# Optimization experiments

Hardware: AMD Instinct MI355X
Metric: run time of the kernel (lower is better)

The kernel has to match this reference:

```python
import jax, jax.numpy as jnp
import numpy as np

WIN = 11      # pytorch_msssim default win_size
SIGMA = 1.5   # pytorch_msssim default win_sigma
K1, K2 = 0.01, 0.03
DATA_RANGE = 1.0


def _gauss_win():
    coords = np.arange(WIN, dtype=np.float64) - WIN // 2
    g = np.exp(-(coords ** 2) / (2.0 * SIGMA ** 2))
    g = g / g.sum()
    return jnp.asarray(g, dtype=jnp.float32)


def _gauss_filter(x, w):
    # x: [B, C, H, W]; separable depthwise gaussian, VALID padding (pytorch_msssim style)
    C = x.shape[1]
    dn = ('NCHW', 'OIHW', 'NCHW')
    kh = jnp.broadcast_to(w.reshape(1, 1, WIN, 1), (C, 1, WIN, 1))
    kw = jnp.broadcast_to(w.reshape(1, 1, 1, WIN), (C, 1, 1, WIN))
    x = jax.lax.conv_general_dilated(x, kh, (1, 1), 'VALID',
                                     dimension_numbers=dn, feature_group_count=C)
    x = jax.lax.conv_general_dilated(x, kw, (1, 1), 'VALID',
                                     dimension_numbers=dn, feature_group_count=C)
    return x


def _ssim_mean(X, Y):
    C1 = (K1 * DATA_RANGE) ** 2
    C2 = (K2 * DATA_RANGE) ** 2
    w = _gauss_win()
    mu1 = _gauss_filter(X, w)
    mu2 = _gauss_filter(Y, w)
    mu1_sq = mu1 * mu1
    mu2_sq = mu2 * mu2
    mu1_mu2 = mu1 * mu2
    sigma1_sq = _gauss_filter(X * X, w) - mu1_sq
    sigma2_sq = _gauss_filter(Y * Y, w) - mu2_sq
    sigma12 = _gauss_filter(X * Y, w) - mu1_mu2
    cs_map = (2.0 * sigma12 + C2) / (sigma1_sq + sigma2_sq + C2)
    ssim_map = ((2.0 * mu1_mu2 + C1) / (mu1_sq + mu2_sq + C1)) * cs_map
    return jnp.mean(ssim_map)


def setup_inputs() -> dict:
    key = jax.random.key(0)
    k1, k2 = jax.random.split(key)
    inp = jax.random.uniform(k1, (64, 1, 512, 512), dtype=jnp.float32)
    tgt = jax.random.uniform(k2, (64, 1, 512, 512), dtype=jnp.float32)
    return {"input": inp, "target": tgt}


def reference(input, target):
    # SSIMLoss.forward: 1 - SSIM(data_range=1, size_average=True, channel=1)(input, target)
    return 1.0 - _ssim_mean(input, target)
```

## Files before the change

kernel.cpp:

```cpp
#include <hip/hip_runtime.h>
#include <math.h>

#define WIN 11
#define OH 32
#define OW 54
#define IWV 64
#define VSTRH 64
#define PLANEH (OH * VSTRH)
#define IMG 512
#define OUTD 502
#define NIMG 64
#define NTX 10

typedef float    f32x2 __attribute__((ext_vector_type(2)));
typedef _Float16 h2    __attribute__((ext_vector_type(2)));
typedef _Float16 h8    __attribute__((ext_vector_type(8)));

struct GW {
    float    wf[WIN];
    unsigned whp[WIN];
};

__device__ inline h2 wsplat(unsigned u) {
    union { unsigned u; h2 h; } x; x.u = u; return x.h;
}

__global__ __launch_bounds__(64) void ssim_zero(double* acc) {
    if (threadIdx.x == 0) acc[0] = 0.0;
}

__global__ __launch_bounds__(256, 4) void ssim_kernel(
    const float* __restrict__ X, const float* __restrict__ Y,
    double* __restrict__ acc, GW gw)
{
    __shared__ _Float16 vb[5 * PLANEH];
    __shared__ float red[4];

    const int tid = threadIdx.x;
    const int tC = blockIdx.x, tR = blockIdx.y, b = blockIdx.z;
    const int gr0 = tR * OH, gc0 = tC * OW;
    const float* __restrict__ Xb = X + (size_t)b * (IMG * IMG);
    const float* __restrict__ Yb = Y + (size_t)b * (IMG * IMG);

    {
        const int rg = tid >> 5, cg = tid & 31;
        const int r0 = rg * 4;
        int gc = gc0 + cg * 2;
        if (gc > IMG - 2) gc = IMG - 2;

        f32x2 a[5][4] = {};
        #pragma unroll
        for (int k = 0; k < 4 + WIN - 1; ++k) {
            int gr = gr0 + r0 + k; if (gr > IMG - 1) gr = IMG - 1;
            const float2 xv = *reinterpret_cast<const float2*>(Xb + (size_t)gr * IMG + gc);
            const float2 yv = *reinterpret_cast<const float2*>(Yb + (size_t)gr * IMG + gc);
            f32x2 x = {xv.x, xv.y};
            f32x2 y = {yv.x, yv.y};
            f32x2 xx = x * x, yy = y * y, xy = x * y;
            #pragma unroll
            for (int i2 = 0; i2 < 4; ++i2) {
                const int t = k - i2;
                if (t >= 0 && t < WIN) {
                    const float wt = gw.wf[t];
                    a[0][i2] += wt * x;
                    a[1][i2] += wt * y;
                    a[2][i2] += wt * xx;
                    a[3][i2] += wt * yy;
                    a[4][i2] += wt * xy;
                }
            }
        }
        #pragma unroll
        for (int ch = 0; ch < 5; ++ch) {
            #pragma unroll
            for (int i2 = 0; i2 < 4; ++i2) {
                h2 hv = { (_Float16)a[ch][i2].x, (_Float16)a[ch][i2].y };
                *reinterpret_cast<h2*>(&vb[ch * PLANEH + (r0 + i2) * VSTRH + cg * 2]) = hv;
            }
        }
    }
    __syncthreads();

    const int r   = tid >> 3;
    const int c0h = (tid & 7) * 8;
    const _Float16* rb = &vb[r * VSTRH];

    const int b1 = (c0h == 56) ? 56 : c0h + 8;
    int b2 = c0h + 16; if (b2 > 62) b2 = 62;

    h2 m[5][4];
    #pragma unroll
    for (int ch = 0; ch < 5; ++ch) {
        const _Float16* p = rb + ch * PLANEH;
        h8 v0 = *reinterpret_cast<const h8*>(p + c0h);
        h8 v1 = *reinterpret_cast<const h8*>(p + b1);
        h2 e8 = *reinterpret_cast<const h2*>(p + b2);
        h2 e[9];
        #pragma unroll
        for (int j = 0; j < 4; ++j) { e[j] = h2{ v0[2*j], v0[2*j+1] }; }
        #pragma unroll
        for (int j = 0; j < 4; ++j) { e[4+j] = h2{ v1[2*j], v1[2*j+1] }; }
        e[8] = e8;
        h2 o[8];
        #pragma unroll
        for (int j = 0; j < 8; ++j) { o[j] = h2{ e[j][1], e[j+1][0] }; }

        #pragma unroll
        for (int pr = 0; pr < 4; ++pr) {
            h2 s = h2{ (_Float16)0, (_Float16)0 };
            #pragma unroll
            for (int u = 0; u < 6; ++u)
                s += wsplat(gw.whp[2*u]) * e[pr + u];
            #pragma unroll
            for (int u = 0; u < 5; ++u)
                s += wsplat(gw.whp[2*u+1]) * o[pr + u];
            m[ch][pr] = s;
        }
    }

    const float C1 = 1e-4f, C2 = 9e-4f;
    int cmax = OUTD - gc0; if (cmax > OW) cmax = OW;
    const int rmax = OUTD - gr0;
    const bool rowok = (r < rmax);

    float lsum = 0.f;
    #pragma unroll
    for (int pr = 0; pr < 4; ++pr) {
        #pragma unroll
        for (int h = 0; h < 2; ++h) {
            float mu1 = (float)m[0][pr][h];
            float mu2 = (float)m[1][pr][h];
            float mu1s = mu1 * mu1, mu2s = mu2 * mu2, m12 = mu1 * mu2;
            float s1  = (float)m[2][pr][h] - mu1s;
            float s2  = (float)m[3][pr][h] - mu2s;
            float s12 = (float)m[4][pr][h] - m12;
            float num = (2.f * s12 + C2) * (2.f * m12 + C1);
            float den = (s1 + s2 + C2) * (mu1s + mu2s + C1);
            float ss  = num * __builtin_amdgcn_rcpf(den);
            if (rowok && (c0h + 2*pr + h) < cmax) lsum += ss;
        }
    }

    #pragma unroll
    for (int off = 32; off > 0; off >>= 1)
        lsum += __shfl_down(lsum, off, 64);
    if ((tid & 63) == 0) red[tid >> 6] = lsum;
    __syncthreads();
    if (tid == 0) {
        float bs = red[0] + red[1] + red[2] + red[3];
        atomicAdd(acc, (double)bs);
    }
}

__global__ void ssim_finalize(const double* __restrict__ acc,
                              float* __restrict__ out) {
    out[0] = 1.0f - (float)(acc[0] / (double)((long long)NIMG * OUTD * OUTD));
}

static unsigned short f2h_rne(float f) {
    union { float f; unsigned u; } v; v.f = f;
    unsigned u = v.u;
    unsigned s = (u >> 16) & 0x8000u;
    int e = (int)((u >> 23) & 0xff) - 112;
    unsigned mant = u & 0x7fffffu;
    unsigned h = s | ((unsigned)e << 10) | (mant >> 13);
    unsigned rem = mant & 0x1fffu;
    if (rem > 0x1000u || (rem == 0x1000u && (h & 1u))) h++;
    return (unsigned short)h;
}

extern "C" void kernel_launch(void* const* d_in, const int* in_sizes, int n_in,
                              void* d_out, int out_size, void* d_ws, size_t ws_size,
                              hipStream_t stream) {
    const float* X = (const float*)d_in[0];
    const float* Y = (const float*)d_in[1];
    double* acc = (double*)d_ws;
    float* out = (float*)d_out;

    GW gw;
    double c[WIN], s = 0.0;
    for (int i = 0; i < WIN; ++i) {
        double d = (double)i - (double)(WIN / 2);
        c[i] = exp(-(d * d) / (2.0 * 1.5 * 1.5));
        s += c[i];
    }
    for (int i = 0; i < WIN; ++i) {
        float w = (float)(c[i] / s);
        gw.wf[i] = w;
        unsigned short hb = f2h_rne(w);
        gw.whp[i] = (unsigned)hb | ((unsigned)hb << 16);
    }

    ssim_zero<<<1, 64, 0, stream>>>(acc);
    dim3 grid(NTX, IMG / OH, NIMG);
    ssim_kernel<<<grid, 256, 0, stream>>>(X, Y, acc, gw);
    ssim_finalize<<<1, 1, 0, stream>>>(acc, out);
}
```

Before: 146.2 us.

## Do vertical gaussian pass in packed fp16 with wider 64-column tiles

The vertical filter pass now converts inputs to packed fp16 and accumulates the five moment planes with packed half FMAs, with each thread loading float4 instead of float2. Tiles widen to 64 output columns (8x16 grid), so 152 of 256 threads do the vertical pass. The shared stride grows to 80 and the launch-bounds occupancy hint drops to 3. Edge masking now runs only on boundary tiles, and the odd-offset pairs are built with a shift-based align. The aim is fewer ALU ops and blocks, at the cost of fp16 accumulation error in the squared moments and idle threads during the first phase.

```diff
diff --git a/kernel.cpp b/kernel.cpp
--- a/kernel.cpp
+++ b/kernel.cpp
@@ -3,33 +3,36 @@
 
 #define WIN 11
 #define OH 32
-#define OW 54
-#define IWV 64
-#define VSTRH 64
+#define OW 64
+#define VSTRH 80
 #define PLANEH (OH * VSTRH)
 #define IMG 512
 #define OUTD 502
 #define NIMG 64
-#define NTX 10
-
-typedef float    f32x2 __attribute__((ext_vector_type(2)));
-typedef _Float16 h2    __attribute__((ext_vector_type(2)));
-typedef _Float16 h8    __attribute__((ext_vector_type(8)));
-
-struct GW {
-    float    wf[WIN];
-    unsigned whp[WIN];
-};
-
-__device__ inline h2 wsplat(unsigned u) {
-    union { unsigned u; h2 h; } x; x.u = u; return x.h;
+
+typedef _Float16 h2 __attribute__((ext_vector_type(2)));
+typedef _Float16 h4 __attribute__((ext_vector_type(4)));
+typedef _Float16 h8 __attribute__((ext_vector_type(8)));
+typedef __fp16   fp16x2 __attribute__((ext_vector_type(2)));
+
+struct GW { unsigned whp[WIN]; };
+
+union U32H2 { unsigned u; h2 h; fp16x2 f; };
+__device__ inline h2 wsplat(unsigned u) { U32H2 x; x.u = u; return x.h; }
+__device__ inline h2 alignh(h2 hi, h2 lo) {
+    U32H2 a, b, r; a.h = lo; b.h = hi;
+    r.u = (a.u >> 16) | (b.u << 16);
+    return r.h;
+}
+__device__ inline h2 pkrtz(float a, float b) {
+    U32H2 x; x.f = __builtin_amdgcn_cvt_pkrtz(a, b); return x.h;
 }
 
 __global__ __launch_bounds__(64) void ssim_zero(double* acc) {
     if (threadIdx.x == 0) acc[0] = 0.0;
 }
 
-__global__ __launch_bounds__(256, 4) void ssim_kernel(
+__global__ __launch_bounds__(256, 3) void ssim_kernel(
     const float* __restrict__ X, const float* __restrict__ Y,
     double* __restrict__ acc, GW gw)
 {
@@ -42,31 +45,35 @@
     const float* __restrict__ Xb = X + (size_t)b * (IMG * IMG);
     const float* __restrict__ Yb = Y + (size_t)b * (IMG * IMG);
 
-    {
-        const int rg = tid >> 5, cg = tid & 31;
+    if (tid < 152) {
+        const int rg = tid / 19, cg = tid - rg * 19;
         const int r0 = rg * 4;
-        int gc = gc0 + cg * 2;
-        if (gc > IMG - 2) gc = IMG - 2;
-
-        f32x2 a[5][4] = {};
+        int gc = gc0 + cg * 4;
+        if (gc > IMG - 4) gc = IMG - 4;
+
+        h2 a[5][4][2] = {};
         #pragma unroll
         for (int k = 0; k < 4 + WIN - 1; ++k) {
             int gr = gr0 + r0 + k; if (gr > IMG - 1) gr = IMG - 1;
-            const float2 xv = *reinterpret_cast<const float2*>(Xb + (size_t)gr * IMG + gc);
-            const float2 yv = *reinterpret_cast<const float2*>(Yb + (size_t)gr * IMG + gc);
-            f32x2 x = {xv.x, xv.y};
-            f32x2 y = {yv.x, yv.y};
-            f32x2 xx = x * x, yy = y * y, xy = x * y;
+            const float4 xv = *reinterpret_cast<const float4*>(Xb + (size_t)gr * IMG + gc);
+            const float4 yv = *reinterpret_cast<const float4*>(Yb + (size_t)gr * IMG + gc);
+            h2 x0 = pkrtz(xv.x, xv.y);
+            h2 x1 = pkrtz(xv.z, xv.w);
+            h2 y0 = pkrtz(yv.x, yv.y);
+            h2 y1 = pkrtz(yv.z, yv.w);
+            h2 xx0 = x0 * x0, xx1 = x1 * x1;
+            h2 yy0 = y0 * y0, yy1 = y1 * y1;
+            h2 xy0 = x0 * y0, xy1 = x1 * y1;
             #pragma unroll
             for (int i2 = 0; i2 < 4; ++i2) {
                 const int t = k - i2;
                 if (t >= 0 && t < WIN) {
-                    const float wt = gw.wf[t];
-                    a[0][i2] += wt * x;
-                    a[1][i2] += wt * y;
-                    a[2][i2] += wt * xx;
-                    a[3][i2] += wt * yy;
-                    a[4][i2] += wt * xy;
+                    const h2 wt = wsplat(gw.whp[t]);
+                    a[0][i2][0] += wt * x0;  a[0][i2][1] += wt * x1;
+                    a[1][i2][0] += wt * y0;  a[1][i2][1] += wt * y1;
+                    a[2][i2][0] += wt * xx0; a[2][i2][1] += wt * xx1;
+                    a[3][i2][0] += wt * yy0; a[3][i2][1] += wt * yy1;
+                    a[4][i2][0] += wt * xy0; a[4][i2][1] += wt * xy1;
                 }
             }
         }
@@ -74,8 +81,10 @@
         for (int ch = 0; ch < 5; ++ch) {
             #pragma unroll
             for (int i2 = 0; i2 < 4; ++i2) {
-                h2 hv = { (_Float16)a[ch][i2].x, (_Float16)a[ch][i2].y };
-                *reinterpret_cast<h2*>(&vb[ch * PLANEH + (r0 + i2) * VSTRH + cg * 2]) = hv;
+                h4 v;
+                v[0] = a[ch][i2][0][0]; v[1] = a[ch][i2][0][1];
+                v[2] = a[ch][i2][1][0]; v[3] = a[ch][i2][1][1];
+                *reinterpret_cast<h4*>(&vb[ch * PLANEH + (r0 + i2) * VSTRH + cg * 4]) = v;
             }
         }
     }
@@ -84,26 +93,23 @@
     const int r   = tid >> 3;
     const int c0h = (tid & 7) * 8;
     const _Float16* rb = &vb[r * VSTRH];
-
-    const int b1 = (c0h == 56) ? 56 : c0h + 8;
-    int b2 = c0h + 16; if (b2 > 62) b2 = 62;
 
     h2 m[5][4];
     #pragma unroll
     for (int ch = 0; ch < 5; ++ch) {
         const _Float16* p = rb + ch * PLANEH;
         h8 v0 = *reinterpret_cast<const h8*>(p + c0h);
-        h8 v1 = *reinterpret_cast<const h8*>(p + b1);
-        h2 e8 = *reinterpret_cast<const h2*>(p + b2);
+        h8 v1 = *reinterpret_cast<const h8*>(p + c0h + 8);
+        h2 e8 = *reinterpret_cast<const h2*>(p + c0h + 16);
         h2 e[9];
         #pragma unroll
-        for (int j = 0; j < 4; ++j) { e[j] = h2{ v0[2*j], v0[2*j+1] }; }
-        #pragma unroll
-        for (int j = 0; j < 4; ++j) { e[4+j] = h2{ v1[2*j], v1[2*j+1] }; }
+        for (int j = 0; j < 4; ++j) e[j]     = h2{ v0[2*j], v0[2*j+1] };
+        #pragma unroll
+        for (int j = 0; j < 4; ++j) e[4 + j] = h2{ v1[2*j], v1[2*j+1] };
         e[8] = e8;
         h2 o[8];
         #pragma unroll
-        for (int j = 0; j < 8; ++j) { o[j] = h2{ e[j][1], e[j+1][0] }; }
+        for (int j = 0; j < 8; ++j) o[j] = alignh(e[j+1], e[j]);
 
         #pragma unroll
         for (int pr = 0; pr < 4; ++pr) {
@@ -119,11 +125,7 @@
     }
 
     const float C1 = 1e-4f, C2 = 9e-4f;
-    int cmax = OUTD - gc0; if (cmax > OW) cmax = OW;
-    const int rmax = OUTD - gr0;
-    const bool rowok = (r < rmax);
-
-    float lsum = 0.f;
+    float ssv[8];
     #pragma unroll
     for (int pr = 0; pr < 4; ++pr) {
         #pragma unroll
@@ -136,8 +138,20 @@
             float s12 = (float)m[4][pr][h] - m12;
             float num = (2.f * s12 + C2) * (2.f * m12 + C1);
             float den = (s1 + s2 + C2) * (mu1s + mu2s + C1);
-            float ss  = num * __builtin_amdgcn_rcpf(den);
-            if (rowok && (c0h + 2*pr + h) < cmax) lsum += ss;
+            ssv[2*pr + h] = num * __builtin_amdgcn_rcpf(den);
+        }
+    }
+
+    float lsum = 0.f;
+    if (tR < 15 && tC < 7) {
+        #pragma unroll
+        for (int o = 0; o < 8; ++o) lsum += ssv[o];
+    } else {
+        const int ogr = gr0 + r;
+        #pragma unroll
+        for (int o = 0; o < 8; ++o) {
+            const int ogc = gc0 + c0h + o;
+            if (ogr < OUTD && ogc < OUTD) lsum += ssv[o];
         }
     }
 
@@ -185,14 +199,12 @@
         s += c[i];
     }
     for (int i = 0; i < WIN; ++i) {
-        float w = (float)(c[i] / s);
-        gw.wf[i] = w;
-        unsigned short hb = f2h_rne(w);
+        unsigned short hb = f2h_rne((float)(c[i] / s));
         gw.whp[i] = (unsigned)hb | ((unsigned)hb << 16);
     }
 
     ssim_zero<<<1, 64, 0, stream>>>(acc);
-    dim3 grid(NTX, IMG / OH, NIMG);
+    dim3 grid(IMG / OW, IMG / OH, NIMG);
     ssim_kernel<<<grid, 256, 0, stream>>>(X, Y, acc, gw);
     ssim_finalize<<<1, 1, 0, stream>>>(acc, out);
 }
```

Result: faster. 124.6 us (-14.8%).
